# Kernel optimization log

Hardware: AMD Instinct MI355X
Metric: run time of the kernel (lower is better)

## Reference

```python
import jax, jax.numpy as jnp
import numpy as np

X_DIM = 40
N_BATCH = 65536


def _circ_conv1d(x, W, b, pad):
    # x: [N, C_in, L], W: [C_out, C_in, K] (torch layout), circular padding
    if pad > 0:
        x = jnp.pad(x, ((0, 0), (0, 0), (pad, pad)), mode='wrap')
    y = jax.lax.conv_general_dilated(x, W, window_strides=(1,), padding='VALID',
                                     dimension_numbers=('NCH', 'OIH', 'NCH'))
    return y + b[None, :, None]


def setup_inputs() -> dict:
    key = jax.random.key(0)
    ks = jax.random.split(key, 9)
    u = jax.random.normal(ks[0], (N_BATCH, X_DIM), dtype=jnp.float32)
    coeff = jax.random.normal(ks[1], (18,), dtype=jnp.float32) * 0.1
    # Conv1d params, torch layout [out_ch, in_ch, kernel], kaiming-ish scale
    W1 = jax.random.normal(ks[2], (72, 1, 5), dtype=jnp.float32) * (1.0 / np.sqrt(1 * 5))
    b1 = jax.random.normal(ks[3], (72,), dtype=jnp.float32) * 0.05
    W2 = jax.random.normal(ks[4], (37, 48, 5), dtype=jnp.float32) * (1.0 / np.sqrt(48 * 5))
    b2 = jax.random.normal(ks[5], (37,), dtype=jnp.float32) * 0.05
    W3 = jax.random.normal(ks[6], (1, 37, 1), dtype=jnp.float32) * (1.0 / np.sqrt(37))
    b3 = jax.random.normal(ks[7], (1,), dtype=jnp.float32) * 0.05
    t = jnp.zeros((1,), dtype=jnp.float32)  # unused by the module, kept for signature fidelity
    return {"t": t, "u": u, "coeff": coeff, "W1": W1, "b1": b1,
            "W2": W2, "b2": b2, "W3": W3, "b3": b3}


def reference(t, u, coeff, W1, b1, W2, b2, W3, b3):
    # circular neighbor gathers: index_select with (i+k)%D == roll by -k
    u_m2 = jnp.roll(u, 2, axis=-1)
    u_m1 = jnp.roll(u, 1, axis=-1)
    u_p1 = jnp.roll(u, -1, axis=-1)
    u_p2 = jnp.roll(u, -2, axis=-1)
    feats = jnp.stack([
        jnp.ones_like(u),
        u_m2, u_m1, u, u_p1, u_p2,
        u_m2 ** 2, u_m1 ** 2, u ** 2, u_p1 ** 2, u_p2 ** 2,
        u_m2 * u_m1, u_m1 * u, u * u_p1, u_p1 * u_p2,
        u_m2 * u, u_m1 * u_p1, u * u_p2,
    ], axis=-1)  # [N, D, 18]
    out1 = feats @ coeff  # [N, D]

    x = u[:, None, :]  # [N, 1, D]
    h = jax.nn.relu(_circ_conv1d(x, W1, b1, 2))  # [N, 72, D]
    h = jnp.concatenate([h[:, :24], h[:, 24:48] * h[:, 48:]], axis=1)  # [N, 48, D]
    h = jax.nn.relu(_circ_conv1d(h, W2, b2, 2))  # [N, 37, D]
    out2 = _circ_conv1d(h, W3, b3, 0)[:, 0, :]  # [N, D]
    return out1 + out2
```

## Files before the change

### kernel.cpp

```cpp
#include <hip/hip_runtime.h>
#include <hip/hip_bf16.h>

typedef short s16x8 __attribute__((ext_vector_type(8)));
typedef short s16x4 __attribute__((ext_vector_type(4)));
typedef float f32x4 __attribute__((ext_vector_type(4)));

#define TB 8
#define NBG 16
#define HALO 46
#define GSTRIDE 2216
#define USTRIDE 50
#define NT 3
#define GT_SHORTS (TB * GSTRIDE)

__device__ __forceinline__ unsigned short f2bf(float f) {
    unsigned int u = __float_as_uint(f);
    u += 0x7fff + ((u >> 16) & 1);
    return (unsigned short)(u >> 16);
}

__device__ __forceinline__ unsigned int pk_bf16(float lo, float hi) {
    float2 f; f.x = lo; f.y = hi;
    __hip_bfloat162 h = __float22bfloat162_rn(f);
    union { __hip_bfloat162 b; unsigned int u; } c;
    c.b = h;
    return c.u;
}

__global__ __launch_bounds__(256, 2) void lorenz96_fused(
    const float* __restrict__ u,
    const float* __restrict__ coeff,
    const float* __restrict__ W1,
    const float* __restrict__ b1,
    const float* __restrict__ W2,
    const float* __restrict__ b2,
    const float* __restrict__ W3,
    const float* __restrict__ b3,
    float* __restrict__ out)
{
    __shared__ __align__(16) unsigned short gtile[2][GT_SHORTS];
    __shared__ __align__(16) float u_sbuf[2][TB * USTRIDE];

    unsigned short* B_lds = &gtile[0][0];

    const int t    = threadIdx.x;
    const int lane = t & 63;
    const int wave = t >> 6;
    const int quad = lane >> 4;
    const int l15  = lane & 15;

    const int b0_block = blockIdx.x * (TB * NBG);

    for (int g = t; g < NT * 8 * 64; g += 256) {
        int lg = g & 63;
        int ks = (g >> 6) & 7;
        int nt = g >> 9;
        int o  = nt * 16 + (lg & 15);
        int kb = ks * 32 + (lg >> 4) * 8;
        s16x8 pack = {0, 0, 0, 0, 0, 0, 0, 0};
        #pragma unroll
        for (int j = 0; j < 8; ++j) {
            int k = kb + j;
            if (o < 37) {
                if (k < 240) {
                    int c = k % 48, tap = k / 48;
                    pack[j] = (short)f2bf(W2[o * 240 + c * 5 + tap]);
                } else if (k == 240) {
                    pack[j] = (short)f2bf(b2[o]);
                }
            }
        }
        *(s16x8*)&B_lds[g * 8] = pack;
    }

    s16x8 aW1[5];
    {
        int chs[5];
        chs[0] = l15; chs[1] = 16 + l15; chs[2] = 32 + l15;
        chs[3] = (l15 >= 8) ? 40 + l15 : -1;
        chs[4] = 56 + l15;
        #pragma unroll
        for (int mt = 0; mt < 5; ++mt) {
            s16x8 a = {0, 0, 0, 0, 0, 0, 0, 0};
            int ch = chs[mt];
            if (quad == 0 && ch >= 0) {
                #pragma unroll
                for (int j = 0; j < 5; ++j) a[j] = (short)f2bf(W1[ch * 5 + j]);
                a[5] = (short)f2bf(b1[ch]);
            }
            aW1[mt] = a;
        }
    }

    float w3v[NT][4];
    #pragma unroll
    for (int nt = 0; nt < NT; ++nt)
        #pragma unroll
        for (int r = 0; r < 4; ++r) {
            int o = nt * 16 + quad * 4 + r;
            w3v[nt][r] = (o < 37) ? W3[o] : 0.f;
        }
    const float b3v = b3[0];
    float cf[18];
    #pragma unroll
    for (int i = 0; i < 18; ++i) cf[i] = coeff[i];

    s16x8 aW2[NT][8];
    float pv_q = 0.f, pv_4 = 0.f;

    auto prestage_u = [&](int grp) {
        for (int idx = t; idx < TB * USTRIDE; idx += 256) {
            int b = idx / USTRIDE, k = idx - b * USTRIDE;
            int gi = k + 36; gi -= (gi >= 40) ? 40 : 0; gi -= (gi >= 40) ? 40 : 0;
            u_sbuf[grp & 1][idx] = u[(size_t)(b0_block + grp * TB + b) * 40 + gi];
        }
    };

    auto poly1 = [&](const float* u_s, int m) -> float {
        int p = m >> 3, b = m & 7;
        const float* us = &u_s[b * USTRIDE + p];
        float um2 = us[2], um1 = us[3], u0 = us[4], up1 = us[5], up2 = us[6];
        return cf[0] + cf[1]*um2 + cf[2]*um1 + cf[3]*u0 + cf[4]*up1 + cf[5]*up2
             + cf[6]*um2*um2 + cf[7]*um1*um1 + cf[8]*u0*u0 + cf[9]*up1*up1 + cf[10]*up2*up2
             + cf[11]*um2*um1 + cf[12]*um1*u0 + cf[13]*u0*up1 + cf[14]*up1*up2
             + cf[15]*um2*u0 + cf[16]*um1*up1 + cf[17]*u0*up2;
    };

    auto poly = [&](int grp) {
        const float* u_s = u_sbuf[grp & 1];
        pv_q = poly1(u_s, (wave + 4 * quad) * 16 + l15);
        pv_4 = poly1(u_s, (wave + 16) * 16 + l15);
    };

    auto phase2 = [&](int grp) {
        const float* u_s = u_sbuf[grp & 1];
        unsigned short* gt = &gtile[grp & 1][0];
        #pragma unroll
        for (int i = 0; i < 6; ++i) {
            const int ct = wave + 4 * i;
            if (ct > 22) continue;
            const int col = ct * 16 + l15;
            const int b = col & 7, h = col >> 3;
            s16x8 bU = {0, 0, 0, 0, 0, 0, 0, 0};
            if (quad == 0) {
                const float* us = &u_s[b * USTRIDE + h];
                union { s16x8 v; unsigned int w[4]; } bu;
                bu.w[0] = pk_bf16(us[0], us[1]);
                bu.w[1] = pk_bf16(us[2], us[3]);
                bu.w[2] = pk_bf16(us[4], 1.0f);
                bu.w[3] = 0;
                bU = bu.v;
            }
            f32x4 a0 = {0.f,0.f,0.f,0.f}, a1 = a0, a2 = a0, a3 = a0, a4 = a0;
            a0 = __builtin_amdgcn_mfma_f32_16x16x32_bf16(aW1[0], bU, a0, 0, 0, 0);
            a1 = __builtin_amdgcn_mfma_f32_16x16x32_bf16(aW1[1], bU, a1, 0, 0, 0);
            a2 = __builtin_amdgcn_mfma_f32_16x16x32_bf16(aW1[2], bU, a2, 0, 0, 0);
            a3 = __builtin_amdgcn_mfma_f32_16x16x32_bf16(aW1[3], bU, a3, 0, 0, 0);
            a4 = __builtin_amdgcn_mfma_f32_16x16x32_bf16(aW1[4], bU, a4, 0, 0, 0);
            float v0[4], v1[4], v2[4];
            #pragma unroll
            for (int r = 0; r < 4; ++r) {
                v0[r] = fmaxf(a0[r], 0.f);
                v1[r] = fmaxf(a1[r], 0.f);
                if (quad >= 2) v1[r] *= fmaxf(a3[r], 0.f);
                v2[r] = fmaxf(a2[r], 0.f) * fmaxf(a4[r], 0.f);
            }
            union { s16x4 v; unsigned int w[2]; } w0, w1, w2;
            w0.w[0] = pk_bf16(v0[0], v0[1]); w0.w[1] = pk_bf16(v0[2], v0[3]);
            w1.w[0] = pk_bf16(v1[0], v1[1]); w1.w[1] = pk_bf16(v1[2], v1[3]);
            w2.w[0] = pk_bf16(v2[0], v2[1]); w2.w[1] = pk_bf16(v2[2], v2[3]);
            unsigned short* gp = &gt[b * GSTRIDE + h * 48 + quad * 4];
            *(s16x4*)(gp)      = w0.v;
            *(s16x4*)(gp + 16) = w1.v;
            *(s16x4*)(gp + 32) = w2.v;
        }
    };

    auto p3_tile = [&](int i, const unsigned short* gt, int b0) {
        const int mt = wave + 4 * i;
        const int m  = mt * 16 + l15;
        const int p  = m >> 3, b = m & 7;
        const unsigned short* gbase = &gt[b * GSTRIDE + p * 48 + quad * 8];
        s16x8 bg[8];
        #pragma unroll
        for (int ks = 0; ks < 8; ++ks) bg[ks] = *(const s16x8*)(gbase + ks * 32);
        {
            s16x8 b7 = bg[7];
            if (quad == 2) b7[0] = (short)0x3F80;
            bg[7] = b7;
        }
        f32x4 c0 = {0.f,0.f,0.f,0.f}, c1 = c0, c2 = c0;
        #pragma unroll
        for (int ks = 0; ks < 8; ++ks) {
            c0 = __builtin_amdgcn_mfma_f32_16x16x32_bf16(aW2[0][ks], bg[ks], c0, 0, 0, 0);
            c1 = __builtin_amdgcn_mfma_f32_16x16x32_bf16(aW2[1][ks], bg[ks], c1, 0, 0, 0);
            c2 = __builtin_amdgcn_mfma_f32_16x16x32_bf16(aW2[2][ks], bg[ks], c2, 0, 0, 0);
        }
        float s = 0.f;
        #pragma unroll
        for (int r = 0; r < 4; ++r) {
            s += fmaxf(c0[r], 0.f) * w3v[0][r];
            s += fmaxf(c1[r], 0.f) * w3v[1][r];
            s += fmaxf(c2[r], 0.f) * w3v[2][r];
        }
        s += __shfl_xor(s, 16, 64);
        s += __shfl_xor(s, 32, 64);
        const float pv = (i < 4) ? pv_q : pv_4;
        const bool  st = (i < 4) ? (quad == i) : (quad == 0);
        if (st) {
            out[(size_t)(b0 + (l15 & 7)) * 40 + 2 * mt + (l15 >> 3)] = s + b3v + pv;
        }
    };

    prestage_u(0);
    __syncthreads();

    #pragma unroll
    for (int nt = 0; nt < NT; ++nt)
        #pragma unroll
        for (int ks = 0; ks < 8; ++ks)
            aW2[nt][ks] = *(const s16x8*)&B_lds[((nt * 8 + ks) * 64 + lane) * 8];

    poly(0);
    prestage_u(1);
    __syncthreads();

    phase2(0);
    __syncthreads();

    for (int g = 0; g < NBG; ++g) {
        const int b0 = b0_block + g * TB;
        const unsigned short* gt = &gtile[g & 1][0];

        #pragma unroll
        for (int i = 0; i < 5; ++i) p3_tile(i, gt, b0);

        if (g + 1 < NBG) {
            poly(g + 1);
            phase2(g + 1);
            if (g + 2 < NBG) prestage_u(g + 2);
            __syncthreads();
        }
    }
}

extern "C" void kernel_launch(void* const* d_in, const int* in_sizes, int n_in,
                              void* d_out, int out_size, void* d_ws, size_t ws_size,
                              hipStream_t stream) {
    const float* u     = (const float*)d_in[1];
    const float* coeff = (const float*)d_in[2];
    const float* W1    = (const float*)d_in[3];
    const float* b1    = (const float*)d_in[4];
    const float* W2    = (const float*)d_in[5];
    const float* b2    = (const float*)d_in[6];
    const float* W3    = (const float*)d_in[7];
    const float* b3    = (const float*)d_in[8];
    float* out = (float*)d_out;

    const int n_batch = in_sizes[1] / 40;
    const int grid = n_batch / (TB * NBG);
    lorenz96_fused<<<grid, 256, 0, stream>>>(u, coeff, W1, b1, W2, b2, W3, b3, out);
}
```

Before: 182.9 us.

## Single-buffer G tile, shrink registers, and raise occupancy to three blocks per CU

The double-buffered LDS G tile becomes a single buffer, with an extra barrier per group so phase3 reads finish before phase2 overwrites it. Launch bounds rise to three blocks per CU and the batch groups per block are halved, giving twice as many blocks. Register pressure drops: the 18 polynomial coefficients are reloaded through a volatile pointer instead of held in registers, the first conv uses the smaller 16x16x16 MFMA with 4-wide operands, and phase3 loads B fragments per k-step instead of all eight up front. The extra sync, the repeated coefficient loads and the loss of load-ahead in phase3 are the costs traded for higher occupancy.

```diff
diff --git a/kernel.cpp b/kernel.cpp
--- a/kernel.cpp
+++ b/kernel.cpp
@@ -6,7 +6,7 @@
 typedef float f32x4 __attribute__((ext_vector_type(4)));
 
 #define TB 8
-#define NBG 16
+#define NBG 8
 #define HALO 46
 #define GSTRIDE 2216
 #define USTRIDE 50
@@ -27,7 +27,7 @@
     return c.u;
 }
 
-__global__ __launch_bounds__(256, 2) void lorenz96_fused(
+__global__ __launch_bounds__(256, 3) void lorenz96_fused(
     const float* __restrict__ u,
     const float* __restrict__ coeff,
     const float* __restrict__ W1,
@@ -38,10 +38,10 @@
     const float* __restrict__ b3,
     float* __restrict__ out)
 {
-    __shared__ __align__(16) unsigned short gtile[2][GT_SHORTS];
+    __shared__ __align__(16) unsigned short gtile[GT_SHORTS];
     __shared__ __align__(16) float u_sbuf[2][TB * USTRIDE];
 
-    unsigned short* B_lds = &gtile[0][0];
+    unsigned short* B_lds = gtile;
 
     const int t    = threadIdx.x;
     const int lane = t & 63;
@@ -73,7 +73,7 @@
         *(s16x8*)&B_lds[g * 8] = pack;
     }
 
-    s16x8 aW1[5];
+    s16x4 aW1[5];
     {
         int chs[5];
         chs[0] = l15; chs[1] = 16 + l15; chs[2] = 32 + l15;
@@ -81,12 +81,16 @@
         chs[4] = 56 + l15;
         #pragma unroll
         for (int mt = 0; mt < 5; ++mt) {
-            s16x8 a = {0, 0, 0, 0, 0, 0, 0, 0};
+            s16x4 a = {0, 0, 0, 0};
             int ch = chs[mt];
-            if (quad == 0 && ch >= 0) {
-                #pragma unroll
-                for (int j = 0; j < 5; ++j) a[j] = (short)f2bf(W1[ch * 5 + j]);
-                a[5] = (short)f2bf(b1[ch]);
+            if (ch >= 0) {
+                if (quad == 0) {
+                    #pragma unroll
+                    for (int j = 0; j < 4; ++j) a[j] = (short)f2bf(W1[ch * 5 + j]);
+                } else if (quad == 1) {
+                    a[0] = (short)f2bf(W1[ch * 5 + 4]);
+                    a[1] = (short)f2bf(b1[ch]);
+                }
             }
             aW1[mt] = a;
         }
@@ -101,9 +105,8 @@
             w3v[nt][r] = (o < 37) ? W3[o] : 0.f;
         }
     const float b3v = b3[0];
-    float cf[18];
-    #pragma unroll
-    for (int i = 0; i < 18; ++i) cf[i] = coeff[i];
+
+    const volatile float* coeffv = (const volatile float*)coeff;
 
     s16x8 aW2[NT][8];
     float pv_q = 0.f, pv_4 = 0.f;
@@ -116,85 +119,94 @@
         }
     };
 
-    auto poly1 = [&](const float* u_s, int m) -> float {
+    auto poly1 = [&](const float* u_s, const float* c, int m) -> float {
         int p = m >> 3, b = m & 7;
         const float* us = &u_s[b * USTRIDE + p];
         float um2 = us[2], um1 = us[3], u0 = us[4], up1 = us[5], up2 = us[6];
-        return cf[0] + cf[1]*um2 + cf[2]*um1 + cf[3]*u0 + cf[4]*up1 + cf[5]*up2
-             + cf[6]*um2*um2 + cf[7]*um1*um1 + cf[8]*u0*u0 + cf[9]*up1*up1 + cf[10]*up2*up2
-             + cf[11]*um2*um1 + cf[12]*um1*u0 + cf[13]*u0*up1 + cf[14]*up1*up2
-             + cf[15]*um2*u0 + cf[16]*um1*up1 + cf[17]*u0*up2;
+        return c[0] + c[1]*um2 + c[2]*um1 + c[3]*u0 + c[4]*up1 + c[5]*up2
+             + c[6]*um2*um2 + c[7]*um1*um1 + c[8]*u0*u0 + c[9]*up1*up1 + c[10]*up2*up2
+             + c[11]*um2*um1 + c[12]*um1*u0 + c[13]*u0*up1 + c[14]*up1*up2
+             + c[15]*um2*u0 + c[16]*um1*up1 + c[17]*u0*up2;
     };
 
     auto poly = [&](int grp) {
+        float c[18];
+        #pragma unroll
+        for (int i = 0; i < 18; ++i) c[i] = coeffv[i];
         const float* u_s = u_sbuf[grp & 1];
-        pv_q = poly1(u_s, (wave + 4 * quad) * 16 + l15);
-        pv_4 = poly1(u_s, (wave + 16) * 16 + l15);
+        pv_q = poly1(u_s, c, (wave + 4 * quad) * 16 + l15);
+        pv_4 = poly1(u_s, c, (wave + 16) * 16 + l15);
     };
 
     auto phase2 = [&](int grp) {
         const float* u_s = u_sbuf[grp & 1];
-        unsigned short* gt = &gtile[grp & 1][0];
         #pragma unroll
         for (int i = 0; i < 6; ++i) {
             const int ct = wave + 4 * i;
             if (ct > 22) continue;
             const int col = ct * 16 + l15;
             const int b = col & 7, h = col >> 3;
-            s16x8 bU = {0, 0, 0, 0, 0, 0, 0, 0};
+            s16x4 bU = {0, 0, 0, 0};
             if (quad == 0) {
                 const float* us = &u_s[b * USTRIDE + h];
-                union { s16x8 v; unsigned int w[4]; } bu;
+                union { s16x4 v; unsigned int w[2]; } bu;
                 bu.w[0] = pk_bf16(us[0], us[1]);
                 bu.w[1] = pk_bf16(us[2], us[3]);
-                bu.w[2] = pk_bf16(us[4], 1.0f);
-                bu.w[3] = 0;
                 bU = bu.v;
-            }
-            f32x4 a0 = {0.f,0.f,0.f,0.f}, a1 = a0, a2 = a0, a3 = a0, a4 = a0;
-            a0 = __builtin_amdgcn_mfma_f32_16x16x32_bf16(aW1[0], bU, a0, 0, 0, 0);
-            a1 = __builtin_amdgcn_mfma_f32_16x16x32_bf16(aW1[1], bU, a1, 0, 0, 0);
-            a2 = __builtin_amdgcn_mfma_f32_16x16x32_bf16(aW1[2], bU, a2, 0, 0, 0);
-            a3 = __builtin_amdgcn_mfma_f32_16x16x32_bf16(aW1[3], bU, a3, 0, 0, 0);
-            a4 = __builtin_amdgcn_mfma_f32_16x16x32_bf16(aW1[4], bU, a4, 0, 0, 0);
-            float v0[4], v1[4], v2[4];
-            #pragma unroll
-            for (int r = 0; r < 4; ++r) {
-                v0[r] = fmaxf(a0[r], 0.f);
-                v1[r] = fmaxf(a1[r], 0.f);
-                if (quad >= 2) v1[r] *= fmaxf(a3[r], 0.f);
-                v2[r] = fmaxf(a2[r], 0.f) * fmaxf(a4[r], 0.f);
-            }
-            union { s16x4 v; unsigned int w[2]; } w0, w1, w2;
-            w0.w[0] = pk_bf16(v0[0], v0[1]); w0.w[1] = pk_bf16(v0[2], v0[3]);
-            w1.w[0] = pk_bf16(v1[0], v1[1]); w1.w[1] = pk_bf16(v1[2], v1[3]);
-            w2.w[0] = pk_bf16(v2[0], v2[1]); w2.w[1] = pk_bf16(v2[2], v2[3]);
-            unsigned short* gp = &gt[b * GSTRIDE + h * 48 + quad * 4];
-            *(s16x4*)(gp)      = w0.v;
-            *(s16x4*)(gp + 16) = w1.v;
-            *(s16x4*)(gp + 32) = w2.v;
-        }
-    };
-
-    auto p3_tile = [&](int i, const unsigned short* gt, int b0) {
+            } else if (quad == 1) {
+                const float* us = &u_s[b * USTRIDE + h];
+                union { s16x4 v; unsigned int w[2]; } bu;
+                bu.w[0] = pk_bf16(us[4], 1.0f);
+                bu.w[1] = 0;
+                bU = bu.v;
+            }
+            unsigned short* gp = &gtile[b * GSTRIDE + h * 48 + quad * 4];
+            {
+                f32x4 a0 = {0.f,0.f,0.f,0.f}, a1 = a0, a3 = a0;
+                a0 = __builtin_amdgcn_mfma_f32_16x16x16bf16_1k(aW1[0], bU, a0, 0, 0, 0);
+                a1 = __builtin_amdgcn_mfma_f32_16x16x16bf16_1k(aW1[1], bU, a1, 0, 0, 0);
+                a3 = __builtin_amdgcn_mfma_f32_16x16x16bf16_1k(aW1[3], bU, a3, 0, 0, 0);
+                float v0[4], v1[4];
+                #pragma unroll
+                for (int r = 0; r < 4; ++r) {
+                    v0[r] = fmaxf(a0[r], 0.f);
+                    v1[r] = fmaxf(a1[r], 0.f);
+                    if (quad >= 2) v1[r] *= fmaxf(a3[r], 0.f);
+                }
+                union { s16x4 v; unsigned int w[2]; } w0, w1;
+                w0.w[0] = pk_bf16(v0[0], v0[1]); w0.w[1] = pk_bf16(v0[2], v0[3]);
+                w1.w[0] = pk_bf16(v1[0], v1[1]); w1.w[1] = pk_bf16(v1[2], v1[3]);
+                *(s16x4*)(gp)      = w0.v;
+                *(s16x4*)(gp + 16) = w1.v;
+            }
+            {
+                f32x4 a2 = {0.f,0.f,0.f,0.f}, a4 = a2;
+                a2 = __builtin_amdgcn_mfma_f32_16x16x16bf16_1k(aW1[2], bU, a2, 0, 0, 0);
+                a4 = __builtin_amdgcn_mfma_f32_16x16x16bf16_1k(aW1[4], bU, a4, 0, 0, 0);
+                float v2[4];
+                #pragma unroll
+                for (int r = 0; r < 4; ++r)
+                    v2[r] = fmaxf(a2[r], 0.f) * fmaxf(a4[r], 0.f);
+                union { s16x4 v; unsigned int w[2]; } w2;
+                w2.w[0] = pk_bf16(v2[0], v2[1]); w2.w[1] = pk_bf16(v2[2], v2[3]);
+                *(s16x4*)(gp + 32) = w2.v;
+            }
+        }
+    };
+
+    auto p3_tile = [&](int i, int b0) {
         const int mt = wave + 4 * i;
         const int m  = mt * 16 + l15;
         const int p  = m >> 3, b = m & 7;
-        const unsigned short* gbase = &gt[b * GSTRIDE + p * 48 + quad * 8];
-        s16x8 bg[8];
-        #pragma unroll
-        for (int ks = 0; ks < 8; ++ks) bg[ks] = *(const s16x8*)(gbase + ks * 32);
-        {
-            s16x8 b7 = bg[7];
-            if (quad == 2) b7[0] = (short)0x3F80;
-            bg[7] = b7;
-        }
+        const unsigned short* gbase = &gtile[b * GSTRIDE + p * 48 + quad * 8];
         f32x4 c0 = {0.f,0.f,0.f,0.f}, c1 = c0, c2 = c0;
         #pragma unroll
         for (int ks = 0; ks < 8; ++ks) {
-            c0 = __builtin_amdgcn_mfma_f32_16x16x32_bf16(aW2[0][ks], bg[ks], c0, 0, 0, 0);
-            c1 = __builtin_amdgcn_mfma_f32_16x16x32_bf16(aW2[1][ks], bg[ks], c1, 0, 0, 0);
-            c2 = __builtin_amdgcn_mfma_f32_16x16x32_bf16(aW2[2][ks], bg[ks], c2, 0, 0, 0);
+            s16x8 bgk = *(const s16x8*)(gbase + ks * 32);
+            if (ks == 7 && quad == 2) bgk[0] = (short)0x3F80;
+            c0 = __builtin_amdgcn_mfma_f32_16x16x32_bf16(aW2[0][ks], bgk, c0, 0, 0, 0);
+            c1 = __builtin_amdgcn_mfma_f32_16x16x32_bf16(aW2[1][ks], bgk, c1, 0, 0, 0);
+            c2 = __builtin_amdgcn_mfma_f32_16x16x32_bf16(aW2[2][ks], bgk, c2, 0, 0, 0);
         }
         float s = 0.f;
         #pragma unroll
@@ -222,20 +234,20 @@
             aW2[nt][ks] = *(const s16x8*)&B_lds[((nt * 8 + ks) * 64 + lane) * 8];
 
     poly(0);
+    __syncthreads();
+
+    phase2(0);
     prestage_u(1);
     __syncthreads();
 
-    phase2(0);
-    __syncthreads();
-
     for (int g = 0; g < NBG; ++g) {
         const int b0 = b0_block + g * TB;
-        const unsigned short* gt = &gtile[g & 1][0];
-
-        #pragma unroll
-        for (int i = 0; i < 5; ++i) p3_tile(i, gt, b0);
+
+        #pragma unroll
+        for (int i = 0; i < 5; ++i) p3_tile(i, b0);
 
         if (g + 1 < NBG) {
+            __syncthreads();
             poly(g + 1);
             phase2(g + 1);
             if (g + 2 < NBG) prestage_u(g + 2);
```

Result: slower. 303.0 us (+65.7%).
